# Optimization experiments

Hardware: AMD Instinct MI355X
Metric: run time of the kernel (lower is better)

Reference implementation:

```python
import jax, jax.numpy as jnp
import numpy as np

B, N, T, H, HEADS, HD, BK, FC, HOR = 8, 1600, 64, 32, 4, 8, 8, 16, 12


def setup_inputs() -> dict:
    key = jax.random.key(0)
    ks = jax.random.split(key, 32)
    r = lambda i, shape, s=0.1: jax.random.normal(ks[i], shape, dtype=jnp.float32) * s
    return dict(
        x=jax.random.normal(ks[0], (B, T, N), dtype=jnp.float32),
        dw_w=r(1, (1, 1, 3)), dw_b=r(2, (1,)),
        bn1_g=jnp.ones((1,), jnp.float32), bn1_b=jnp.zeros((1,), jnp.float32),
        bn1_m=jnp.zeros((1,), jnp.float32), bn1_v=jnp.ones((1,), jnp.float32),
        pw_w=r(3, (FC, 1, 1)), pw_b=r(4, (FC,)),
        bn2_g=jnp.ones((FC,), jnp.float32), bn2_b=jnp.zeros((FC,), jnp.float32),
        bn2_m=jnp.zeros((FC,), jnp.float32), bn2_v=jnp.ones((FC,), jnp.float32),
        fp_w=r(5, (H, FC * T)), fp_b=r(6, (H,)),
        qkv_lo_w=r(7, (3 * BK, H)), qkv_lo_b=r(8, (3 * BK,)),
        qkv_hi_w=r(9, (3 * H, 3 * BK)), qkv_hi_b=r(10, (3 * H,)),
        out_lo_w=r(11, (BK, H)), out_lo_b=r(12, (BK,)),
        out_hi_w=r(13, (H, BK)), out_hi_b=r(14, (H,)),
        u=r(15, (HEADS, N, BK)), v=r(16, (HEADS, BK, N)),
        log_reg=jnp.float32(np.log(1e-5)),
        hp_w=r(17, (BK, H)), hp_b=r(18, (BK,)),
        gru_wih=r(19, (3 * BK, 1)), gru_whh=r(20, (3 * BK, BK)),
        gru_bih=r(21, (3 * BK,)), gru_bhh=r(22, (3 * BK,)),
        op_w=r(23, (1, BK)), op_b=r(24, (1,)),
        log_decay=jnp.float32(-2.3),
        rg1_w=r(25, (BK, H)), rg1_b=r(26, (BK,)),
        rg2_w=r(27, (HOR, BK)), rg2_b=r(28, (HOR,)),
    )


def _bn(x, g, b, m, v):  # x: [BN, C, T], inference-mode BatchNorm1d
    inv = g / jnp.sqrt(v + 1e-5)
    return (x - m[None, :, None]) * inv[None, :, None] + b[None, :, None]


def _conv1d(x, w, b, pad):
    y = jax.lax.conv_general_dilated(x, w, (1,), [(pad, pad)],
                                     dimension_numbers=('NCH', 'OIH', 'NCH'))
    return y + b[None, :, None]


def reference(x, dw_w, dw_b, bn1_g, bn1_b, bn1_m, bn1_v, pw_w, pw_b,
              bn2_g, bn2_b, bn2_m, bn2_v, fp_w, fp_b,
              qkv_lo_w, qkv_lo_b, qkv_hi_w, qkv_hi_b,
              out_lo_w, out_lo_b, out_hi_w, out_hi_b, u, v, log_reg,
              hp_w, hp_b, gru_wih, gru_whh, gru_bih, gru_bhh, op_w, op_b,
              log_decay, rg1_w, rg1_b, rg2_w, rg2_b):
    # ---- TFEM: depthwise-separable conv per node series (eval mode, dropout off) ----
    xt = x.transpose(0, 2, 1).reshape(B * N, 1, T)          # [BN, 1, T]
    y = jax.nn.relu(_bn(_conv1d(xt, dw_w, dw_b, 1), bn1_g, bn1_b, bn1_m, bn1_v))
    y = jax.nn.relu(_bn(_conv1d(y, pw_w, pw_b, 0), bn2_g, bn2_b, bn2_m, bn2_v))  # [BN, FC, T]
    feat = (y.reshape(B * N, FC * T) @ fp_w.T + fp_b).reshape(B, N, H)

    # ---- LR-AGAM: low-rank qkv, linear attention + dense softmax for reg loss ----
    qkv = (feat @ qkv_lo_w.T + qkv_lo_b) @ qkv_hi_w.T + qkv_hi_b  # [B, N, 3H]
    q, k, vv = jnp.split(qkv, 3, axis=-1)
    resh = lambda t: t.reshape(B, N, HEADS, HD).transpose(0, 2, 1, 3)  # [B, h, N, d]
    q, k, vv = resh(q), resh(k), resh(vv)
    qe = jax.nn.elu(q) + 1.0
    ke = jax.nn.elu(k) + 1.0
    kv = jnp.einsum('bhnd,bhne->bhde', ke, vv)
    z = 1.0 / (ke.sum(-1) + 1e-8)                            # [B, h, N]
    att_out = jnp.einsum('bhnd,bhde,bhn->bhne', qe, kv, z)   # [B, h, N, d]
    # dense scores use the PRE-elu q, k (torch reassigns q/k only locally)
    scores = jnp.einsum('bhnd,bhmd->bhnm', q, k) / np.float32(np.sqrt(HD))
    scores = scores + jnp.matmul(u, v)[None]                 # learnable graph bias
    attn = jax.nn.softmax(scores, axis=-1)
    reg = jnp.exp(log_reg) * jnp.mean(jnp.abs(attn))
    out = att_out.transpose(0, 2, 1, 3).reshape(B, N, H)
    out = (out @ out_lo_w.T + out_lo_b) @ out_hi_w.T + out_hi_b
    feat = feat + out                                        # residual

    last = x[:, -1, :]                                       # [B, N]
    h0 = feat.reshape(B * N, H) @ hp_w.T + hp_b              # [BN, BK]
    cur0 = last.reshape(B * N, 1)

    def step(carry, _):
        h, cur = carry
        gx = cur @ gru_wih.T + gru_bih                       # [BN, 3BK]
        gh = h @ gru_whh.T + gru_bhh
        r_ = jax.nn.sigmoid(gx[:, :BK] + gh[:, :BK])
        zg = jax.nn.sigmoid(gx[:, BK:2 * BK] + gh[:, BK:2 * BK])
        n_ = jnp.tanh(gx[:, 2 * BK:] + r_ * gh[:, 2 * BK:])
        h2 = (1.0 - zg) * n_ + zg * h
        p = h2 @ op_w.T + op_b                               # [BN, 1]
        return (h2, p), p[:, 0]

    _, preds = jax.lax.scan(step, (h0, cur0), None, length=HOR)  # [HOR, BN]
    gru_pred = preds.T.reshape(B, N, HOR)

    gate = jax.nn.sigmoid(jax.nn.relu(feat @ rg1_w.T + rg1_b) @ rg2_w.T + rg2_b)  # [B, N, HOR]
    ts = jnp.arange(1, HOR + 1, dtype=jnp.float32)
    decay = jnp.exp(-jnp.exp(log_decay) * ts)[None, None, :]
    final = gate * gru_pred + (1.0 - gate) * last[..., None] * decay
    return final, reg
```

## Files before the change

### kernel.cpp

```cpp
#include <hip/hip_runtime.h>
#include <math.h>

constexpr int cB = 8, cN = 1600, cT = 64, cH = 32, cHEADS = 4, cHD = 8, cFC = 16, cHOR = 12;
constexpr int cROWS = cB * cN;

typedef __attribute__((ext_vector_type(8))) short short8;
typedef __attribute__((ext_vector_type(4))) float f32x4;

__device__ __forceinline__ float sigmoidf_(float x) { return 1.0f / (1.0f + __expf(-x)); }
__device__ __forceinline__ float tanhf_(float x) {
    float xc = fminf(fmaxf(x, -15.0f), 15.0f);
    float e = __expf(-2.0f * xc);
    return (1.0f - e) / (1.0f + e);
}
__device__ __forceinline__ float elu1_(float x) { return (x > 0.0f) ? (x + 1.0f) : __expf(x); }
__device__ __forceinline__ short f2bf(float f) {
    unsigned u = __float_as_uint(f);
    u = (u + 0x7fffu + ((u >> 16) & 1u)) >> 16;
    return (short)u;
}

__global__ __launch_bounds__(256) void k0_init(const float* __restrict__ fp_w,
                                               unsigned short* __restrict__ wbt,
                                               float* __restrict__ kv) {
    int i = blockIdx.x * 256 + threadIdx.x;
    wbt[i] = (unsigned short)f2bf(fp_w[i]);
    if (i < cB * cHEADS * 64) kv[i] = 0.0f;
}

__global__ __launch_bounds__(64) void kFeat(
    const float* __restrict__ x,
    const float* __restrict__ dw_w, const float* __restrict__ dw_b,
    const float* __restrict__ bn1_g, const float* __restrict__ bn1_b,
    const float* __restrict__ bn1_m, const float* __restrict__ bn1_v,
    const float* __restrict__ pw_w, const float* __restrict__ pw_b,
    const float* __restrict__ bn2_g, const float* __restrict__ bn2_b,
    const float* __restrict__ bn2_m, const float* __restrict__ bn2_v,
    const unsigned short* __restrict__ wbt,
    float* __restrict__ feat_p)
{
    __shared__ float y1s[16 * 65];

    const int l = threadIdx.x;
    const int rg = blockIdx.x >> 1;
    const int hk = blockIdx.x & 1;
    const int r0 = rg * 16;
    const int b = r0 / cN;
    const int n0 = r0 - b * cN;

    const float inv1 = bn1_g[0] * rsqrtf(bn1_v[0] + 1e-5f);
    const float A = inv1;
    const float C = (dw_b[0] - bn1_m[0]) * inv1 + bn1_b[0];
    const float w0 = dw_w[0], w1 = dw_w[1], w2 = dw_w[2];

    {
        const int rr = l & 15;
        const int t0 = (l >> 4) * 16;
        const float* xp = x + (size_t)b * cT * cN + (n0 + rr);
        float xv[18];
        #pragma unroll
        for (int q = 0; q < 18; ++q) {
            int t = t0 - 1 + q;
            xv[q] = (t >= 0 && t < cT) ? xp[(size_t)t * cN] : 0.0f;
        }
        #pragma unroll
        for (int q = 0; q < 16; ++q) {
            float s = w0 * xv[q] + w1 * xv[q + 1] + w2 * xv[q + 2];
            y1s[rr * 65 + t0 + q] = fmaxf(0.0f, fmaf(s, A, C));
        }
    }
    __syncthreads();

    float a2r[8], c2r[8];
    #pragma unroll
    for (int cc = 0; cc < 8; ++cc) {
        const int c = hk * 8 + cc;
        const float inv2 = bn2_g[c] * rsqrtf(bn2_v[c] + 1e-5f);
        a2r[cc] = pw_w[c] * inv2;
        c2r[cc] = (pw_b[c] - bn2_m[c]) * inv2 + bn2_b[c];
    }

    const int rr = l & 15;
    const int off = (l >> 4) * 8;
    float y1r[16];
    #pragma unroll
    for (int p = 0; p < 8; ++p) {
        y1r[p]     = y1s[rr * 65 + off + p];
        y1r[8 + p] = y1s[rr * 65 + 32 + off + p];
    }

    const unsigned short* b0p = wbt + (size_t)(l & 15) * 1024 + hk * 512 + off;
    const unsigned short* b1p = wbt + (size_t)(16 + (l & 15)) * 1024 + hk * 512 + off;

    f32x4 acc0 = {0.f, 0.f, 0.f, 0.f};
    f32x4 acc1 = {0.f, 0.f, 0.f, 0.f};

    #pragma unroll
    for (int kk = 0; kk < 16; ++kk) {
        const float a2 = a2r[kk >> 1], c2v = c2r[kk >> 1];
        short8 af;
        #pragma unroll
        for (int i = 0; i < 8; ++i) {
            const float y2 = fmaxf(0.0f, fmaf(a2, y1r[(kk & 1) * 8 + i], c2v));
            af[i] = f2bf(y2);
        }
        const short8 bf0 = *(const short8*)(b0p + kk * 32);
        const short8 bf1 = *(const short8*)(b1p + kk * 32);
        acc0 = __builtin_amdgcn_mfma_f32_16x16x32_bf16(af, bf0, acc0, 0, 0, 0);
        acc1 = __builtin_amdgcn_mfma_f32_16x16x32_bf16(af, bf1, acc1, 0, 0, 0);
    }

    float* fp = feat_p + (size_t)hk * ((size_t)cROWS * cH);
    const int col = l & 15;
    const int rbase = r0 + (l >> 4) * 4;
    #pragma unroll
    for (int reg = 0; reg < 4; ++reg) {
        fp[(size_t)(rbase + reg) * cH + col]      = acc0[reg];
        fp[(size_t)(rbase + reg) * cH + 16 + col] = acc1[reg];
    }
}

__global__ __launch_bounds__(256) void k2_qkv(
    const float* __restrict__ feat_p, const float* __restrict__ fp_b,
    const float* __restrict__ lo_w, const float* __restrict__ lo_b,
    const float* __restrict__ hi_w, const float* __restrict__ hi_b,
    float* __restrict__ feat_c, float* __restrict__ qe,
    float* __restrict__ zz, float* __restrict__ kvout)
{
    __shared__ float lbuf[32][25];
    __shared__ float ske[32][33];
    __shared__ float svv[32][33];

    const int tid = threadIdx.x;
    const int r = tid >> 3;
    const int j = tid & 7;
    const int row = blockIdx.x * 32 + r;
    const int b = __builtin_amdgcn_readfirstlane((blockIdx.x * 32) / cN);
    const int n = row - b * cN;

    float f[cH];
    {
        const float4* f0 = (const float4*)(feat_p + (size_t)row * cH);
        const float4* f1 = (const float4*)(feat_p + (size_t)cROWS * cH + (size_t)row * cH);
        #pragma unroll
        for (int q = 0; q < 8; ++q) {
            float4 v0 = f0[q], v1 = f1[q];
            f[4*q]   = v0.x + v1.x + fp_b[4*q];
            f[4*q+1] = v0.y + v1.y + fp_b[4*q+1];
            f[4*q+2] = v0.z + v1.z + fp_b[4*q+2];
            f[4*q+3] = v0.w + v1.w + fp_b[4*q+3];
        }
    }
    {
        float4 wc;
        wc.x = f[4*j]; wc.y = f[4*j+1]; wc.z = f[4*j+2]; wc.w = f[4*j+3];
        ((float4*)(feat_c + (size_t)row * cH))[j] = wc;
    }

    float lo0 = lo_b[j], lo1 = lo_b[j+8], lo2 = lo_b[j+16];
    #pragma unroll
    for (int i = 0; i < cH; ++i) {
        lo0 = fmaf(f[i], lo_w[j * cH + i], lo0);
        lo1 = fmaf(f[i], lo_w[(j+8) * cH + i], lo1);
        lo2 = fmaf(f[i], lo_w[(j+16) * cH + i], lo2);
    }
    lbuf[r][j] = lo0; lbuf[r][j+8] = lo1; lbuf[r][j+16] = lo2;
    __syncthreads();
    float lof[24];
    #pragma unroll
    for (int i = 0; i < 24; ++i) lof[i] = lbuf[r][i];

    float qv[4], kv4[4], vv4[4];
    #pragma unroll
    for (int m = 0; m < 4; ++m) {
        const int oi = m * 8 + j;
        float sq = hi_b[oi], sk = hi_b[32 + oi], sv = hi_b[64 + oi];
        #pragma unroll
        for (int i = 0; i < 24; ++i) {
            sq = fmaf(lof[i], hi_w[oi * 24 + i], sq);
            sk = fmaf(lof[i], hi_w[(32 + oi) * 24 + i], sk);
            sv = fmaf(lof[i], hi_w[(64 + oi) * 24 + i], sv);
        }
        qv[m] = elu1_(sq);
        kv4[m] = elu1_(sk);
        vv4[m] = sv;
    }

    float s0 = kv4[0], s1 = kv4[1], s2 = kv4[2], s3 = kv4[3];
    #pragma unroll
    for (int off = 1; off < 8; off <<= 1) {
        s0 += __shfl_xor(s0, off, 8);
        s1 += __shfl_xor(s1, off, 8);
        s2 += __shfl_xor(s2, off, 8);
        s3 += __shfl_xor(s3, off, 8);
    }
    if (j < 4) {
        float sv = (j == 0) ? s0 : ((j == 1) ? s1 : ((j == 2) ? s2 : s3));
        zz[(size_t)(b * cHEADS + j) * cN + n] = 1.0f / (sv + 1e-8f);
    }

    #pragma unroll
    for (int m = 0; m < 4; ++m) {
        qe[(size_t)row * cH + m * 8 + j] = qv[m];
        ske[r][m * 8 + j] = kv4[m];
        svv[r][m * 8 + j] = vv4[m];
    }
    __syncthreads();

    {
        const int m = tid >> 6, d = (tid >> 3) & 7, e = tid & 7;
        float s = 0.0f;
        #pragma unroll
        for (int rr = 0; rr < 32; ++rr)
            s = fmaf(ske[rr][m * 8 + d], svv[rr][m * 8 + e], s);
        atomicAdd(&kvout[(size_t)(b * cHEADS + m) * 64 + d * 8 + e], s);
    }
}

__global__ __launch_bounds__(256) void k4_final(
    const float* __restrict__ x,
    const float* __restrict__ feat_c, const float* __restrict__ qe,
    const float* __restrict__ zz, const float* __restrict__ kv,
    const float* __restrict__ out_lo_w, const float* __restrict__ out_lo_b,
    const float* __restrict__ out_hi_w, const float* __restrict__ out_hi_b,
    const float* __restrict__ hp_w, const float* __restrict__ hp_b,
    const float* __restrict__ gru_wih, const float* __restrict__ gru_whh,
    const float* __restrict__ gru_bih, const float* __restrict__ gru_bhh,
    const float* __restrict__ op_w, const float* __restrict__ op_b,
    const float* __restrict__ log_decay,
    const float* __restrict__ rg1_w, const float* __restrict__ rg1_b,
    const float* __restrict__ rg2_w, const float* __restrict__ rg2_b,
    const float* __restrict__ log_reg,
    float* __restrict__ out)
{
    __shared__ float sA[32][36];
    __shared__ float sB[32][36];
    __shared__ float sC[32][36];

    const int tid = threadIdx.x;
    const int r = tid >> 3;
    const int j = tid & 7;
    const int row = blockIdx.x * 32 + r;
    const int b = __builtin_amdgcn_readfirstlane((blockIdx.x * 32) / cN);
    const int n = row - b * cN;

    {
        const float4* q4 = (const float4*)(qe + (size_t)row * cH);
        float4 v = q4[j];
        *(float4*)&sA[r][4 * j] = v;
    }
    __syncthreads();

    float o_m[4];
    #pragma unroll
    for (int m = 0; m < 4; ++m) {
        const float z = zz[(size_t)(b * cHEADS + m) * cN + n];
        const float* kvp = kv + (size_t)(b * cHEADS + m) * 64;
        float s = 0.0f;
        #pragma unroll
        for (int d = 0; d < 8; ++d)
            s = fmaf(sA[r][m * 8 + d], kvp[d * 8 + j], s);
        o_m[m] = s * z;
    }
    #pragma unroll
    for (int m = 0; m < 4; ++m) sB[r][m * 8 + j] = o_m[m];
    __syncthreads();

    float lo_j = out_lo_b[j];
    #pragma unroll
    for (int i = 0; i < cH; ++i)
        lo_j = fmaf(sB[r][i], out_lo_w[j * cH + i], lo_j);

    float lof[8];
    #pragma unroll
    for (int i = 0; i < 8; ++i) lof[i] = __shfl(lo_j, i, 8);

    float f2_m[4];
    #pragma unroll
    for (int m = 0; m < 4; ++m) {
        const int i = m * 8 + j;
        float s = out_hi_b[i];
        #pragma unroll
        for (int q = 0; q < 8; ++q) s = fmaf(lof[q], out_hi_w[i * 8 + q], s);
        f2_m[m] = feat_c[(size_t)row * cH + i] + s;
        sC[r][i] = f2_m[m];
    }
    __syncthreads();

    float h0_j = hp_b[j], g1_j = rg1_b[j];
    #pragma unroll
    for (int i = 0; i < cH; ++i) {
        float fv = sC[r][i];
        h0_j = fmaf(fv, hp_w[j * cH + i], h0_j);
        g1_j = fmaf(fv, rg1_w[j * cH + i], g1_j);
    }
    g1_j = fmaxf(0.0f, g1_j);

    float g1f[8];
    #pragma unroll
    for (int i = 0; i < 8; ++i) g1f[i] = __shfl(g1_j, i, 8);

    float ga = rg2_b[j], gb_ = rg2_b[8 + (j & 3)];
    #pragma unroll
    for (int q = 0; q < 8; ++q) {
        ga = fmaf(g1f[q], rg2_w[j * 8 + q], ga);
        gb_ = fmaf(g1f[q], rg2_w[(8 + (j & 3)) * 8 + q], gb_);
    }
    const float gate_a = sigmoidf_(ga);
    const float gate_b = sigmoidf_(gb_);

    const float last = x[(size_t)b * cT * cN + (size_t)(cT - 1) * cN + n];

    float whh_r[8], whh_z[8], whh_n[8], opw[8];
    #pragma unroll
    for (int i = 0; i < 8; ++i) {
        whh_r[i] = gru_whh[j * 8 + i];
        whh_z[i] = gru_whh[(8 + j) * 8 + i];
        whh_n[i] = gru_whh[(16 + j) * 8 + i];
        opw[i] = op_w[i];
    }
    const float wih_r = gru_wih[j], wih_z = gru_wih[8 + j], wih_n = gru_wih[16 + j];
    const float bih_r = gru_bih[j], bih_z = gru_bih[8 + j], bih_n = gru_bih[16 + j];
    const float bhh_r = gru_bhh[j], bhh_z = gru_bhh[8 + j], bhh_n = gru_bhh[16 + j];
    const float opb = op_b[0];

    float h_full[8];
    #pragma unroll
    for (int i = 0; i < 8; ++i) h_full[i] = __shfl(h0_j, i, 8);
    float h_own = h0_j;
    float cur = last;
    float po_a = 0.0f, po_b = 0.0f;

    #pragma unroll
    for (int s = 0; s < cHOR; ++s) {
        float ghr = bhh_r, ghz = bhh_z, ghn = bhh_n;
        #pragma unroll
        for (int i = 0; i < 8; ++i) {
            ghr = fmaf(h_full[i], whh_r[i], ghr);
            ghz = fmaf(h_full[i], whh_z[i], ghz);
            ghn = fmaf(h_full[i], whh_n[i], ghn);
        }
        const float r_ = sigmoidf_(fmaf(wih_r, cur, bih_r) + ghr);
        const float zg = sigmoidf_(fmaf(wih_z, cur, bih_z) + ghz);
        const float nn = tanhf_(fmaf(wih_n, cur, bih_n) + r_ * ghn);
        const float hn = (1.0f - zg) * nn + zg * h_own;
        h_own = hn;
        #pragma unroll
        for (int i = 0; i < 8; ++i) h_full[i] = __shfl(hn, i, 8);
        float p = opb;
        #pragma unroll
        for (int i = 0; i < 8; ++i) p = fmaf(h_full[i], opw[i], p);
        po_a = (s == j) ? p : po_a;
        po_b = (s == 8 + j) ? p : po_b;
        cur = p;
    }

    const float dk = __expf(log_decay[0]);
    float* orow = out + (size_t)row * 12;
    orow[j] = gate_a * po_a + (1.0f - gate_a) * last * __expf(-dk * (float)(j + 1));
    if (j < 4)
        orow[8 + j] = gate_b * po_b + (1.0f - gate_b) * last * __expf(-dk * (float)(j + 9));

    if (row == 0 && j == 0)
        out[(size_t)cROWS * 12] = __expf(log_reg[0]) * (1.0f / (float)cN);
}

extern "C" void kernel_launch(void* const* d_in, const int* in_sizes, int n_in,
                              void* d_out, int out_size, void* d_ws, size_t ws_size,
                              hipStream_t stream)
{
    const float* x      = (const float*)d_in[0];
    const float* dw_w   = (const float*)d_in[1];
    const float* dw_b   = (const float*)d_in[2];
    const float* bn1_g  = (const float*)d_in[3];
    const float* bn1_b  = (const float*)d_in[4];
    const float* bn1_m  = (const float*)d_in[5];
    const float* bn1_v  = (const float*)d_in[6];
    const float* pw_w   = (const float*)d_in[7];
    const float* pw_b   = (const float*)d_in[8];
    const float* bn2_g  = (const float*)d_in[9];
    const float* bn2_b  = (const float*)d_in[10];
    const float* bn2_m  = (const float*)d_in[11];
    const float* bn2_v  = (const float*)d_in[12];
    const float* fp_w   = (const float*)d_in[13];
    const float* fp_b   = (const float*)d_in[14];
    const float* lo_w   = (const float*)d_in[15];
    const float* lo_b   = (const float*)d_in[16];
    const float* hi_w   = (const float*)d_in[17];
    const float* hi_b   = (const float*)d_in[18];
    const float* olo_w  = (const float*)d_in[19];
    const float* olo_b  = (const float*)d_in[20];
    const float* ohi_w  = (const float*)d_in[21];
    const float* ohi_b  = (const float*)d_in[22];
    const float* log_reg = (const float*)d_in[25];
    const float* hp_w   = (const float*)d_in[26];
    const float* hp_b   = (const float*)d_in[27];
    const float* gru_wih = (const float*)d_in[28];
    const float* gru_whh = (const float*)d_in[29];
    const float* gru_bih = (const float*)d_in[30];
    const float* gru_bhh = (const float*)d_in[31];
    const float* op_w   = (const float*)d_in[32];
    const float* op_b   = (const float*)d_in[33];
    const float* log_decay = (const float*)d_in[34];
    const float* rg1_w  = (const float*)d_in[35];
    const float* rg1_b  = (const float*)d_in[36];
    const float* rg2_w  = (const float*)d_in[37];
    const float* rg2_b  = (const float*)d_in[38];

    float* ws = (float*)d_ws;
    unsigned short* wbt = (unsigned short*)ws;
    float* feat_p = ws + 16384;
    float* feat_c = feat_p + 2 * 409600;
    float* qe     = feat_c + 409600;
    float* zz     = qe + 409600;
    float* kv     = zz + 51200;

    k0_init<<<128, 256, 0, stream>>>(fp_w, wbt, kv);
    kFeat<<<1600, 64, 0, stream>>>(x, dw_w, dw_b, bn1_g, bn1_b, bn1_m, bn1_v,
                                   pw_w, pw_b, bn2_g, bn2_b, bn2_m, bn2_v,
                                   wbt, feat_p);
    k2_qkv<<<cROWS / 32, 256, 0, stream>>>(feat_p, fp_b, lo_w, lo_b, hi_w, hi_b,
                                           feat_c, qe, zz, kv);
    k4_final<<<cROWS / 32, 256, 0, stream>>>(x, feat_c, qe, zz, kv,
                                             olo_w, olo_b, ohi_w, ohi_b,
                                             hp_w, hp_b, gru_wih, gru_whh, gru_bih, gru_bhh,
                                             op_w, op_b, log_decay,
                                             rg1_w, rg1_b, rg2_w, rg2_b, log_reg,
                                             (float*)d_out);
}
```

Baseline: 52.16 us.

## Fuse feature projection with QKV, fold low-rank weights, replace atomics with reduction

Merges the feature GEMM and the QKV stage into one kernel. Each 16-row block now runs the full K=1024 itself instead of writing split-K partials, which removes the feat_p round trip. The low-rank weight pairs (qkv lo/hi and out lo/hi) are precomputed into dense 96x32 and 32x32 matrices in a prep kernel, and the normalizer z is folded into q. Per-block KV partial sums go to a buffer and are reduced by a small dedicated kernel instead of atomics. The trade-off is half as many blocks in the MFMA kernel, a longer serial K loop, and one extra launch.

```diff
diff --git a/kernel.cpp b/kernel.cpp
--- a/kernel.cpp
+++ b/kernel.cpp
@@ -20,15 +20,51 @@
     return (short)u;
 }
 
-__global__ __launch_bounds__(256) void k0_init(const float* __restrict__ fp_w,
-                                               unsigned short* __restrict__ wbt,
-                                               float* __restrict__ kv) {
-    int i = blockIdx.x * 256 + threadIdx.x;
-    wbt[i] = (unsigned short)f2bf(fp_w[i]);
-    if (i < cB * cHEADS * 64) kv[i] = 0.0f;
-}
-
-__global__ __launch_bounds__(64) void kFeat(
+__global__ __launch_bounds__(256) void k0_prep(
+    const float* __restrict__ fp_w,
+    const float* __restrict__ lo_w, const float* __restrict__ lo_b,
+    const float* __restrict__ hi_w, const float* __restrict__ hi_b,
+    const float* __restrict__ olo_w, const float* __restrict__ olo_b,
+    const float* __restrict__ ohi_w, const float* __restrict__ ohi_b,
+    unsigned short* __restrict__ wbt,
+    float* __restrict__ Wq, float* __restrict__ bq,
+    float* __restrict__ Wo, float* __restrict__ bo)
+{
+    const int g = blockIdx.x * 256 + threadIdx.x;
+    #pragma unroll
+    for (int q = 0; q < 8; ++q) {
+        const int i = g * 8 + q;
+        wbt[i] = (unsigned short)f2bf(fp_w[i]);
+    }
+    if (g < 3072) {
+        const int oi = g >> 5, i = g & 31;
+        float s = 0.0f;
+        #pragma unroll
+        for (int p = 0; p < 24; ++p) s = fmaf(hi_w[oi * 24 + p], lo_w[p * 32 + i], s);
+        Wq[g] = s;
+    }
+    if (g < 1024) {
+        const int i = g >> 5, q = g & 31;
+        float s = 0.0f;
+        #pragma unroll
+        for (int p = 0; p < 8; ++p) s = fmaf(ohi_w[i * 8 + p], olo_w[p * 32 + q], s);
+        Wo[g] = s;
+    }
+    if (g < 96) {
+        float s = hi_b[g];
+        #pragma unroll
+        for (int p = 0; p < 24; ++p) s = fmaf(hi_w[g * 24 + p], lo_b[p], s);
+        bq[g] = s;
+    }
+    if (g < 32) {
+        float s = ohi_b[g];
+        #pragma unroll
+        for (int p = 0; p < 8; ++p) s = fmaf(ohi_w[g * 8 + p], olo_b[p], s);
+        bo[g] = s;
+    }
+}
+
+__global__ __launch_bounds__(64) void kFQ(
     const float* __restrict__ x,
     const float* __restrict__ dw_w, const float* __restrict__ dw_b,
     const float* __restrict__ bn1_g, const float* __restrict__ bn1_b,
@@ -36,15 +72,19 @@
     const float* __restrict__ pw_w, const float* __restrict__ pw_b,
     const float* __restrict__ bn2_g, const float* __restrict__ bn2_b,
     const float* __restrict__ bn2_m, const float* __restrict__ bn2_v,
-    const unsigned short* __restrict__ wbt,
-    float* __restrict__ feat_p)
+    const unsigned short* __restrict__ wbt, const float* __restrict__ fp_b,
+    const float* __restrict__ Wq, const float* __restrict__ bq,
+    float* __restrict__ feat_c, float* __restrict__ qe,
+    float* __restrict__ pkv)
 {
     __shared__ float y1s[16 * 65];
+    __shared__ float sfeat[16 * 36];
+    __shared__ float ske[16 * 33];
+    __shared__ float svv[16 * 33];
 
     const int l = threadIdx.x;
-    const int rg = blockIdx.x >> 1;
-    const int hk = blockIdx.x & 1;
-    const int r0 = rg * 16;
+    const int bk = blockIdx.x;
+    const int r0 = bk * 16;
     const int b = r0 / cN;
     const int n0 = r0 - b * cN;
 
@@ -71,13 +111,12 @@
     }
     __syncthreads();
 
-    float a2r[8], c2r[8];
-    #pragma unroll
-    for (int cc = 0; cc < 8; ++cc) {
-        const int c = hk * 8 + cc;
+    float a2r[16], c2r[16];
+    #pragma unroll
+    for (int c = 0; c < 16; ++c) {
         const float inv2 = bn2_g[c] * rsqrtf(bn2_v[c] + 1e-5f);
-        a2r[cc] = pw_w[c] * inv2;
-        c2r[cc] = (pw_b[c] - bn2_m[c]) * inv2 + bn2_b[c];
+        a2r[c] = pw_w[c] * inv2;
+        c2r[c] = (pw_b[c] - bn2_m[c]) * inv2 + bn2_b[c];
     }
 
     const int rr = l & 15;
@@ -89,14 +128,14 @@
         y1r[8 + p] = y1s[rr * 65 + 32 + off + p];
     }
 
-    const unsigned short* b0p = wbt + (size_t)(l & 15) * 1024 + hk * 512 + off;
-    const unsigned short* b1p = wbt + (size_t)(16 + (l & 15)) * 1024 + hk * 512 + off;
+    const unsigned short* b0p = wbt + (size_t)(l & 15) * 1024 + off;
+    const unsigned short* b1p = wbt + (size_t)(16 + (l & 15)) * 1024 + off;
 
     f32x4 acc0 = {0.f, 0.f, 0.f, 0.f};
     f32x4 acc1 = {0.f, 0.f, 0.f, 0.f};
 
     #pragma unroll
-    for (int kk = 0; kk < 16; ++kk) {
+    for (int kk = 0; kk < 32; ++kk) {
         const float a2 = a2r[kk >> 1], c2v = c2r[kk >> 1];
         short8 af;
         #pragma unroll
@@ -110,119 +149,110 @@
         acc1 = __builtin_amdgcn_mfma_f32_16x16x32_bf16(af, bf1, acc1, 0, 0, 0);
     }
 
-    float* fp = feat_p + (size_t)hk * ((size_t)cROWS * cH);
-    const int col = l & 15;
-    const int rbase = r0 + (l >> 4) * 4;
-    #pragma unroll
-    for (int reg = 0; reg < 4; ++reg) {
-        fp[(size_t)(rbase + reg) * cH + col]      = acc0[reg];
-        fp[(size_t)(rbase + reg) * cH + 16 + col] = acc1[reg];
-    }
-}
-
-__global__ __launch_bounds__(256) void k2_qkv(
-    const float* __restrict__ feat_p, const float* __restrict__ fp_b,
-    const float* __restrict__ lo_w, const float* __restrict__ lo_b,
-    const float* __restrict__ hi_w, const float* __restrict__ hi_b,
-    float* __restrict__ feat_c, float* __restrict__ qe,
-    float* __restrict__ zz, float* __restrict__ kvout)
+    {
+        const int col = l & 15;
+        const int rb = (l >> 4) * 4;
+        const float fb0 = fp_b[col], fb1 = fp_b[16 + col];
+        #pragma unroll
+        for (int reg = 0; reg < 4; ++reg) {
+            sfeat[(rb + reg) * 36 + col]      = acc0[reg] + fb0;
+            sfeat[(rb + reg) * 36 + 16 + col] = acc1[reg] + fb1;
+        }
+    }
+    __syncthreads();
+
+    {
+        float v[8];
+        #pragma unroll
+        for (int q = 0; q < 8; ++q)
+            v[q] = sfeat[(l >> 2) * 36 + (l & 3) * 8 + q];
+        float4* dst = (float4*)(feat_c + (size_t)r0 * cH + l * 8);
+        dst[0] = make_float4(v[0], v[1], v[2], v[3]);
+        dst[1] = make_float4(v[4], v[5], v[6], v[7]);
+    }
+
+    {
+        const int rr2 = l >> 2, hd = l & 3;
+        const int row = r0 + rr2;
+        float4 f4[8];
+        #pragma unroll
+        for (int c = 0; c < 8; ++c)
+            f4[c] = *(const float4*)&sfeat[rr2 * 36 + c * 4];
+
+        float qv[8], kev[8], vvv[8];
+        #pragma unroll
+        for (int g = 0; g < 3; ++g) {
+            #pragma unroll
+            for (int jj = 0; jj < 8; ++jj) {
+                const int oi = g * 32 + hd * 8 + jj;
+                const float4* w4 = (const float4*)(Wq + (size_t)oi * 32);
+                float s = bq[oi];
+                #pragma unroll
+                for (int c = 0; c < 8; ++c) {
+                    float4 wv = w4[c];
+                    s = fmaf(f4[c].x, wv.x, s);
+                    s = fmaf(f4[c].y, wv.y, s);
+                    s = fmaf(f4[c].z, wv.z, s);
+                    s = fmaf(f4[c].w, wv.w, s);
+                }
+                if (g == 0) qv[jj] = s;
+                else if (g == 1) kev[jj] = s;
+                else vvv[jj] = s;
+            }
+        }
+        float zsum = 1e-8f;
+        #pragma unroll
+        for (int jj = 0; jj < 8; ++jj) {
+            qv[jj] = elu1_(qv[jj]);
+            kev[jj] = elu1_(kev[jj]);
+            zsum += kev[jj];
+        }
+        const float z = 1.0f / zsum;
+        float4* qdst = (float4*)(qe + (size_t)row * cH + hd * 8);
+        qdst[0] = make_float4(qv[0]*z, qv[1]*z, qv[2]*z, qv[3]*z);
+        qdst[1] = make_float4(qv[4]*z, qv[5]*z, qv[6]*z, qv[7]*z);
+        #pragma unroll
+        for (int jj = 0; jj < 8; ++jj) {
+            ske[rr2 * 33 + hd * 8 + jj] = kev[jj];
+            svv[rr2 * 33 + hd * 8 + jj] = vvv[jj];
+        }
+    }
+    __syncthreads();
+
+    {
+        float out4[4];
+        #pragma unroll
+        for (int j = 0; j < 4; ++j) {
+            const int cc = l * 4 + j;
+            const int h = cc >> 6, d = (cc >> 3) & 7, e = cc & 7;
+            float s = 0.0f;
+            #pragma unroll
+            for (int rr3 = 0; rr3 < 16; ++rr3)
+                s = fmaf(ske[rr3 * 33 + h * 8 + d], svv[rr3 * 33 + h * 8 + e], s);
+            out4[j] = s;
+        }
+        *(float4*)(pkv + (size_t)bk * 256 + l * 4) =
+            make_float4(out4[0], out4[1], out4[2], out4[3]);
+    }
+}
+
+__global__ __launch_bounds__(64) void k3r(const float* __restrict__ pkv,
+                                          float* __restrict__ kv)
 {
-    __shared__ float lbuf[32][25];
-    __shared__ float ske[32][33];
-    __shared__ float svv[32][33];
-
+    const int bh = blockIdx.x;
+    const int b = bh >> 2, h = bh & 3;
     const int tid = threadIdx.x;
-    const int r = tid >> 3;
-    const int j = tid & 7;
-    const int row = blockIdx.x * 32 + r;
-    const int b = __builtin_amdgcn_readfirstlane((blockIdx.x * 32) / cN);
-    const int n = row - b * cN;
-
-    float f[cH];
-    {
-        const float4* f0 = (const float4*)(feat_p + (size_t)row * cH);
-        const float4* f1 = (const float4*)(feat_p + (size_t)cROWS * cH + (size_t)row * cH);
-        #pragma unroll
-        for (int q = 0; q < 8; ++q) {
-            float4 v0 = f0[q], v1 = f1[q];
-            f[4*q]   = v0.x + v1.x + fp_b[4*q];
-            f[4*q+1] = v0.y + v1.y + fp_b[4*q+1];
-            f[4*q+2] = v0.z + v1.z + fp_b[4*q+2];
-            f[4*q+3] = v0.w + v1.w + fp_b[4*q+3];
-        }
-    }
-    {
-        float4 wc;
-        wc.x = f[4*j]; wc.y = f[4*j+1]; wc.z = f[4*j+2]; wc.w = f[4*j+3];
-        ((float4*)(feat_c + (size_t)row * cH))[j] = wc;
-    }
-
-    float lo0 = lo_b[j], lo1 = lo_b[j+8], lo2 = lo_b[j+16];
-    #pragma unroll
-    for (int i = 0; i < cH; ++i) {
-        lo0 = fmaf(f[i], lo_w[j * cH + i], lo0);
-        lo1 = fmaf(f[i], lo_w[(j+8) * cH + i], lo1);
-        lo2 = fmaf(f[i], lo_w[(j+16) * cH + i], lo2);
-    }
-    lbuf[r][j] = lo0; lbuf[r][j+8] = lo1; lbuf[r][j+16] = lo2;
-    __syncthreads();
-    float lof[24];
-    #pragma unroll
-    for (int i = 0; i < 24; ++i) lof[i] = lbuf[r][i];
-
-    float qv[4], kv4[4], vv4[4];
-    #pragma unroll
-    for (int m = 0; m < 4; ++m) {
-        const int oi = m * 8 + j;
-        float sq = hi_b[oi], sk = hi_b[32 + oi], sv = hi_b[64 + oi];
-        #pragma unroll
-        for (int i = 0; i < 24; ++i) {
-            sq = fmaf(lof[i], hi_w[oi * 24 + i], sq);
-            sk = fmaf(lof[i], hi_w[(32 + oi) * 24 + i], sk);
-            sv = fmaf(lof[i], hi_w[(64 + oi) * 24 + i], sv);
-        }
-        qv[m] = elu1_(sq);
-        kv4[m] = elu1_(sk);
-        vv4[m] = sv;
-    }
-
-    float s0 = kv4[0], s1 = kv4[1], s2 = kv4[2], s3 = kv4[3];
-    #pragma unroll
-    for (int off = 1; off < 8; off <<= 1) {
-        s0 += __shfl_xor(s0, off, 8);
-        s1 += __shfl_xor(s1, off, 8);
-        s2 += __shfl_xor(s2, off, 8);
-        s3 += __shfl_xor(s3, off, 8);
-    }
-    if (j < 4) {
-        float sv = (j == 0) ? s0 : ((j == 1) ? s1 : ((j == 2) ? s2 : s3));
-        zz[(size_t)(b * cHEADS + j) * cN + n] = 1.0f / (sv + 1e-8f);
-    }
-
-    #pragma unroll
-    for (int m = 0; m < 4; ++m) {
-        qe[(size_t)row * cH + m * 8 + j] = qv[m];
-        ske[r][m * 8 + j] = kv4[m];
-        svv[r][m * 8 + j] = vv4[m];
-    }
-    __syncthreads();
-
-    {
-        const int m = tid >> 6, d = (tid >> 3) & 7, e = tid & 7;
-        float s = 0.0f;
-        #pragma unroll
-        for (int rr = 0; rr < 32; ++rr)
-            s = fmaf(ske[rr][m * 8 + d], svv[rr][m * 8 + e], s);
-        atomicAdd(&kvout[(size_t)(b * cHEADS + m) * 64 + d * 8 + e], s);
-    }
+    float s = 0.0f;
+    for (int p = 0; p < 100; ++p)
+        s += pkv[(size_t)(b * 100 + p) * 256 + h * 64 + tid];
+    kv[(size_t)bh * 64 + tid] = s;
 }
 
 __global__ __launch_bounds__(256) void k4_final(
     const float* __restrict__ x,
     const float* __restrict__ feat_c, const float* __restrict__ qe,
-    const float* __restrict__ zz, const float* __restrict__ kv,
-    const float* __restrict__ out_lo_w, const float* __restrict__ out_lo_b,
-    const float* __restrict__ out_hi_w, const float* __restrict__ out_hi_b,
+    const float* __restrict__ kv,
+    const float* __restrict__ Wo, const float* __restrict__ bo,
     const float* __restrict__ hp_w, const float* __restrict__ hp_b,
     const float* __restrict__ gru_wih, const float* __restrict__ gru_whh,
     const float* __restrict__ gru_bih, const float* __restrict__ gru_bhh,
@@ -254,34 +284,25 @@
     float o_m[4];
     #pragma unroll
     for (int m = 0; m < 4; ++m) {
-        const float z = zz[(size_t)(b * cHEADS + m) * cN + n];
         const float* kvp = kv + (size_t)(b * cHEADS + m) * 64;
         float s = 0.0f;
         #pragma unroll
         for (int d = 0; d < 8; ++d)
             s = fmaf(sA[r][m * 8 + d], kvp[d * 8 + j], s);
-        o_m[m] = s * z;
+        o_m[m] = s;
     }
     #pragma unroll
     for (int m = 0; m < 4; ++m) sB[r][m * 8 + j] = o_m[m];
     __syncthreads();
-
-    float lo_j = out_lo_b[j];
-    #pragma unroll
-    for (int i = 0; i < cH; ++i)
-        lo_j = fmaf(sB[r][i], out_lo_w[j * cH + i], lo_j);
-
-    float lof[8];
-    #pragma unroll
-    for (int i = 0; i < 8; ++i) lof[i] = __shfl(lo_j, i, 8);
 
     float f2_m[4];
     #pragma unroll
     for (int m = 0; m < 4; ++m) {
         const int i = m * 8 + j;
-        float s = out_hi_b[i];
-        #pragma unroll
-        for (int q = 0; q < 8; ++q) s = fmaf(lof[q], out_hi_w[i * 8 + q], s);
+        float s = bo[i];
+        const float* wrow = Wo + (size_t)i * 32;
+        #pragma unroll
+        for (int q = 0; q < 32; ++q) s = fmaf(sB[r][q], wrow[q], s);
         f2_m[m] = feat_c[(size_t)row * cH + i] + s;
         sC[r][i] = f2_m[m];
     }
@@ -409,20 +430,25 @@
 
     float* ws = (float*)d_ws;
     unsigned short* wbt = (unsigned short*)ws;
-    float* feat_p = ws + 16384;
-    float* feat_c = feat_p + 2 * 409600;
-    float* qe     = feat_c + 409600;
-    float* zz     = qe + 409600;
-    float* kv     = zz + 51200;
-
-    k0_init<<<128, 256, 0, stream>>>(fp_w, wbt, kv);
-    kFeat<<<1600, 64, 0, stream>>>(x, dw_w, dw_b, bn1_g, bn1_b, bn1_m, bn1_v,
-                                   pw_w, pw_b, bn2_g, bn2_b, bn2_m, bn2_v,
-                                   wbt, feat_p);
-    k2_qkv<<<cROWS / 32, 256, 0, stream>>>(feat_p, fp_b, lo_w, lo_b, hi_w, hi_b,
-                                           feat_c, qe, zz, kv);
-    k4_final<<<cROWS / 32, 256, 0, stream>>>(x, feat_c, qe, zz, kv,
-                                             olo_w, olo_b, ohi_w, ohi_b,
+    float* Wq     = ws + 16384;
+    float* bq     = Wq + 3072;
+    float* Wo     = bq + 128;
+    float* bo     = Wo + 1024;
+    float* qe     = bo + 64;
+    float* feat_c = qe + 409600;
+    float* pkv    = feat_c + 409600;
+    float* kv     = pkv + 204800;
+
+    k0_prep<<<16, 256, 0, stream>>>(fp_w, lo_w, lo_b, hi_w, hi_b,
+                                    olo_w, olo_b, ohi_w, ohi_b,
+                                    wbt, Wq, bq, Wo, bo);
+    kFQ<<<800, 64, 0, stream>>>(x, dw_w, dw_b, bn1_g, bn1_b, bn1_m, bn1_v,
+                                pw_w, pw_b, bn2_g, bn2_b, bn2_m, bn2_v,
+                                wbt, fp_b, Wq, bq,
+                                feat_c, qe, pkv);
+    k3r<<<32, 64, 0, stream>>>(pkv, kv);
+    k4_final<<<cROWS / 32, 256, 0, stream>>>(x, feat_c, qe, kv,
+                                             Wo, bo,
                                              hp_w, hp_b, gru_wih, gru_whh, gru_bih, gru_bhh,
                                              op_w, op_b, log_decay,
                                              rg1_w, rg1_b, rg2_w, rg2_b, log_reg,
```

New measurement: 65.54 us. 25.7% more time.

## Fuse all stages into one persistent kernel with grid-wide barrier for KV reduction

Applied to the files above, without the earlier changes.

Replaces the four-kernel pipeline with a single kernel of 400 blocks that keeps each block's 32 rows of features, q, k and v in LDS instead of global memory. The per-batch KV sum is now built from per-block partials followed by an atomic-counter grid barrier, replacing the global atomicAdd and a separate launch. The low-rank weight pairs (qkv lo/hi, out lo/hi) are folded algebraically into single 32-wide matrices inside each block, and the z normalisation is folded into q. Each block now reconverts the full fp_w matrix to bf16 in LDS, which is redundant per-block work, and the grid barrier relies on all 400 blocks being co-resident (two per CU at 74 KB LDS).

```diff
diff --git a/kernel.cpp b/kernel.cpp
--- a/kernel.cpp
+++ b/kernel.cpp
@@ -1,8 +1,11 @@
 #include <hip/hip_runtime.h>
 #include <math.h>
 
-constexpr int cB = 8, cN = 1600, cT = 64, cH = 32, cHEADS = 4, cHD = 8, cFC = 16, cHOR = 12;
+constexpr int cB = 8, cN = 1600, cT = 64, cH = 32, cHEADS = 4, cHOR = 12;
 constexpr int cROWS = cB * cN;
+constexpr int NB = 400;
+constexpr int RPB = 32;
+constexpr int BPB = 50;
 
 typedef __attribute__((ext_vector_type(8))) short short8;
 typedef __attribute__((ext_vector_type(4))) float f32x4;
@@ -20,15 +23,9 @@
     return (short)u;
 }
 
-__global__ __launch_bounds__(256) void k0_init(const float* __restrict__ fp_w,
-                                               unsigned short* __restrict__ wbt,
-                                               float* __restrict__ kv) {
-    int i = blockIdx.x * 256 + threadIdx.x;
-    wbt[i] = (unsigned short)f2bf(fp_w[i]);
-    if (i < cB * cHEADS * 64) kv[i] = 0.0f;
-}
-
-__global__ __launch_bounds__(64) void kFeat(
+#define LDS_BYTES 74368
+
+__global__ __launch_bounds__(256, 2) void mono(
     const float* __restrict__ x,
     const float* __restrict__ dw_w, const float* __restrict__ dw_b,
     const float* __restrict__ bn1_g, const float* __restrict__ bn1_b,
@@ -36,193 +33,11 @@
     const float* __restrict__ pw_w, const float* __restrict__ pw_b,
     const float* __restrict__ bn2_g, const float* __restrict__ bn2_b,
     const float* __restrict__ bn2_m, const float* __restrict__ bn2_v,
-    const unsigned short* __restrict__ wbt,
-    float* __restrict__ feat_p)
-{
-    __shared__ float y1s[16 * 65];
-
-    const int l = threadIdx.x;
-    const int rg = blockIdx.x >> 1;
-    const int hk = blockIdx.x & 1;
-    const int r0 = rg * 16;
-    const int b = r0 / cN;
-    const int n0 = r0 - b * cN;
-
-    const float inv1 = bn1_g[0] * rsqrtf(bn1_v[0] + 1e-5f);
-    const float A = inv1;
-    const float C = (dw_b[0] - bn1_m[0]) * inv1 + bn1_b[0];
-    const float w0 = dw_w[0], w1 = dw_w[1], w2 = dw_w[2];
-
-    {
-        const int rr = l & 15;
-        const int t0 = (l >> 4) * 16;
-        const float* xp = x + (size_t)b * cT * cN + (n0 + rr);
-        float xv[18];
-        #pragma unroll
-        for (int q = 0; q < 18; ++q) {
-            int t = t0 - 1 + q;
-            xv[q] = (t >= 0 && t < cT) ? xp[(size_t)t * cN] : 0.0f;
-        }
-        #pragma unroll
-        for (int q = 0; q < 16; ++q) {
-            float s = w0 * xv[q] + w1 * xv[q + 1] + w2 * xv[q + 2];
-            y1s[rr * 65 + t0 + q] = fmaxf(0.0f, fmaf(s, A, C));
-        }
-    }
-    __syncthreads();
-
-    float a2r[8], c2r[8];
-    #pragma unroll
-    for (int cc = 0; cc < 8; ++cc) {
-        const int c = hk * 8 + cc;
-        const float inv2 = bn2_g[c] * rsqrtf(bn2_v[c] + 1e-5f);
-        a2r[cc] = pw_w[c] * inv2;
-        c2r[cc] = (pw_b[c] - bn2_m[c]) * inv2 + bn2_b[c];
-    }
-
-    const int rr = l & 15;
-    const int off = (l >> 4) * 8;
-    float y1r[16];
-    #pragma unroll
-    for (int p = 0; p < 8; ++p) {
-        y1r[p]     = y1s[rr * 65 + off + p];
-        y1r[8 + p] = y1s[rr * 65 + 32 + off + p];
-    }
-
-    const unsigned short* b0p = wbt + (size_t)(l & 15) * 1024 + hk * 512 + off;
-    const unsigned short* b1p = wbt + (size_t)(16 + (l & 15)) * 1024 + hk * 512 + off;
-
-    f32x4 acc0 = {0.f, 0.f, 0.f, 0.f};
-    f32x4 acc1 = {0.f, 0.f, 0.f, 0.f};
-
-    #pragma unroll
-    for (int kk = 0; kk < 16; ++kk) {
-        const float a2 = a2r[kk >> 1], c2v = c2r[kk >> 1];
-        short8 af;
-        #pragma unroll
-        for (int i = 0; i < 8; ++i) {
-            const float y2 = fmaxf(0.0f, fmaf(a2, y1r[(kk & 1) * 8 + i], c2v));
-            af[i] = f2bf(y2);
-        }
-        const short8 bf0 = *(const short8*)(b0p + kk * 32);
-        const short8 bf1 = *(const short8*)(b1p + kk * 32);
-        acc0 = __builtin_amdgcn_mfma_f32_16x16x32_bf16(af, bf0, acc0, 0, 0, 0);
-        acc1 = __builtin_amdgcn_mfma_f32_16x16x32_bf16(af, bf1, acc1, 0, 0, 0);
-    }
-
-    float* fp = feat_p + (size_t)hk * ((size_t)cROWS * cH);
-    const int col = l & 15;
-    const int rbase = r0 + (l >> 4) * 4;
-    #pragma unroll
-    for (int reg = 0; reg < 4; ++reg) {
-        fp[(size_t)(rbase + reg) * cH + col]      = acc0[reg];
-        fp[(size_t)(rbase + reg) * cH + 16 + col] = acc1[reg];
-    }
-}
-
-__global__ __launch_bounds__(256) void k2_qkv(
-    const float* __restrict__ feat_p, const float* __restrict__ fp_b,
+    const float* __restrict__ fp_w, const float* __restrict__ fp_b,
     const float* __restrict__ lo_w, const float* __restrict__ lo_b,
     const float* __restrict__ hi_w, const float* __restrict__ hi_b,
-    float* __restrict__ feat_c, float* __restrict__ qe,
-    float* __restrict__ zz, float* __restrict__ kvout)
-{
-    __shared__ float lbuf[32][25];
-    __shared__ float ske[32][33];
-    __shared__ float svv[32][33];
-
-    const int tid = threadIdx.x;
-    const int r = tid >> 3;
-    const int j = tid & 7;
-    const int row = blockIdx.x * 32 + r;
-    const int b = __builtin_amdgcn_readfirstlane((blockIdx.x * 32) / cN);
-    const int n = row - b * cN;
-
-    float f[cH];
-    {
-        const float4* f0 = (const float4*)(feat_p + (size_t)row * cH);
-        const float4* f1 = (const float4*)(feat_p + (size_t)cROWS * cH + (size_t)row * cH);
-        #pragma unroll
-        for (int q = 0; q < 8; ++q) {
-            float4 v0 = f0[q], v1 = f1[q];
-            f[4*q]   = v0.x + v1.x + fp_b[4*q];
-            f[4*q+1] = v0.y + v1.y + fp_b[4*q+1];
-            f[4*q+2] = v0.z + v1.z + fp_b[4*q+2];
-            f[4*q+3] = v0.w + v1.w + fp_b[4*q+3];
-        }
-    }
-    {
-        float4 wc;
-        wc.x = f[4*j]; wc.y = f[4*j+1]; wc.z = f[4*j+2]; wc.w = f[4*j+3];
-        ((float4*)(feat_c + (size_t)row * cH))[j] = wc;
-    }
-
-    float lo0 = lo_b[j], lo1 = lo_b[j+8], lo2 = lo_b[j+16];
-    #pragma unroll
-    for (int i = 0; i < cH; ++i) {
-        lo0 = fmaf(f[i], lo_w[j * cH + i], lo0);
-        lo1 = fmaf(f[i], lo_w[(j+8) * cH + i], lo1);
-        lo2 = fmaf(f[i], lo_w[(j+16) * cH + i], lo2);
-    }
-    lbuf[r][j] = lo0; lbuf[r][j+8] = lo1; lbuf[r][j+16] = lo2;
-    __syncthreads();
-    float lof[24];
-    #pragma unroll
-    for (int i = 0; i < 24; ++i) lof[i] = lbuf[r][i];
-
-    float qv[4], kv4[4], vv4[4];
-    #pragma unroll
-    for (int m = 0; m < 4; ++m) {
-        const int oi = m * 8 + j;
-        float sq = hi_b[oi], sk = hi_b[32 + oi], sv = hi_b[64 + oi];
-        #pragma unroll
-        for (int i = 0; i < 24; ++i) {
-            sq = fmaf(lof[i], hi_w[oi * 24 + i], sq);
-            sk = fmaf(lof[i], hi_w[(32 + oi) * 24 + i], sk);
-            sv = fmaf(lof[i], hi_w[(64 + oi) * 24 + i], sv);
-        }
-        qv[m] = elu1_(sq);
-        kv4[m] = elu1_(sk);
-        vv4[m] = sv;
-    }
-
-    float s0 = kv4[0], s1 = kv4[1], s2 = kv4[2], s3 = kv4[3];
-    #pragma unroll
-    for (int off = 1; off < 8; off <<= 1) {
-        s0 += __shfl_xor(s0, off, 8);
-        s1 += __shfl_xor(s1, off, 8);
-        s2 += __shfl_xor(s2, off, 8);
-        s3 += __shfl_xor(s3, off, 8);
-    }
-    if (j < 4) {
-        float sv = (j == 0) ? s0 : ((j == 1) ? s1 : ((j == 2) ? s2 : s3));
-        zz[(size_t)(b * cHEADS + j) * cN + n] = 1.0f / (sv + 1e-8f);
-    }
-
-    #pragma unroll
-    for (int m = 0; m < 4; ++m) {
-        qe[(size_t)row * cH + m * 8 + j] = qv[m];
-        ske[r][m * 8 + j] = kv4[m];
-        svv[r][m * 8 + j] = vv4[m];
-    }
-    __syncthreads();
-
-    {
-        const int m = tid >> 6, d = (tid >> 3) & 7, e = tid & 7;
-        float s = 0.0f;
-        #pragma unroll
-        for (int rr = 0; rr < 32; ++rr)
-            s = fmaf(ske[rr][m * 8 + d], svv[rr][m * 8 + e], s);
-        atomicAdd(&kvout[(size_t)(b * cHEADS + m) * 64 + d * 8 + e], s);
-    }
-}
-
-__global__ __launch_bounds__(256) void k4_final(
-    const float* __restrict__ x,
-    const float* __restrict__ feat_c, const float* __restrict__ qe,
-    const float* __restrict__ zz, const float* __restrict__ kv,
-    const float* __restrict__ out_lo_w, const float* __restrict__ out_lo_b,
-    const float* __restrict__ out_hi_w, const float* __restrict__ out_hi_b,
+    const float* __restrict__ olo_w, const float* __restrict__ olo_b,
+    const float* __restrict__ ohi_w, const float* __restrict__ ohi_b,
     const float* __restrict__ hp_w, const float* __restrict__ hp_b,
     const float* __restrict__ gru_wih, const float* __restrict__ gru_whh,
     const float* __restrict__ gru_bih, const float* __restrict__ gru_bhh,
@@ -231,66 +46,266 @@
     const float* __restrict__ rg1_w, const float* __restrict__ rg1_b,
     const float* __restrict__ rg2_w, const float* __restrict__ rg2_b,
     const float* __restrict__ log_reg,
+    float* __restrict__ pkv, unsigned* __restrict__ cnt,
     float* __restrict__ out)
 {
-    __shared__ float sA[32][36];
-    __shared__ float sB[32][36];
-    __shared__ float sC[32][36];
+    __shared__ __align__(16) unsigned char smem_[LDS_BYTES];
+    short* wbt  = (short*)smem_;
+    float* y1s  = (float*)(smem_ + 66048);
+    float* sfeat = y1s;
+    float* Wq  = (float*)smem_;
+    float* bq  = Wq + 3168;
+    float* Wo  = bq + 96;
+    float* bo  = Wo + 1056;
+    float* qe  = bo + 32;
+    float* ske = qe + 1056;
+    float* svv = ske + 1056;
+    float* skv = svv + 1056;
+    float* sB  = skv + 256;
+    float* sC  = sB + 1152;
 
     const int tid = threadIdx.x;
+    const int bk = blockIdx.x;
+    const int r0 = bk * RPB;
+    const int b = __builtin_amdgcn_readfirstlane(r0 / cN);
+    const int n0 = r0 - b * cN;
+
+    #pragma unroll 4
+    for (int q = 0; q < 32; ++q) {
+        const float4 v = *(const float4*)(fp_w + (size_t)q * 1024 + tid * 4);
+        short* d = wbt + q * 1032 + tid * 4;
+        d[0] = f2bf(v.x); d[1] = f2bf(v.y); d[2] = f2bf(v.z); d[3] = f2bf(v.w);
+    }
+    {
+        const float inv1 = bn1_g[0] * rsqrtf(bn1_v[0] + 1e-5f);
+        const float A = inv1;
+        const float C = (dw_b[0] - bn1_m[0]) * inv1 + bn1_b[0];
+        const float w0 = dw_w[0], w1 = dw_w[1], w2 = dw_w[2];
+        const int rr = tid & 31;
+        const int t0 = (tid >> 5) * 8;
+        const float* xp = x + (size_t)b * cT * cN + (n0 + rr);
+        float xv[10];
+        #pragma unroll
+        for (int q = 0; q < 10; ++q) {
+            const int t = t0 - 1 + q;
+            xv[q] = (t >= 0 && t < cT) ? xp[(size_t)t * cN] : 0.0f;
+        }
+        #pragma unroll
+        for (int q = 0; q < 8; ++q) {
+            const float s = w0 * xv[q] + w1 * xv[q + 1] + w2 * xv[q + 2];
+            y1s[rr * 65 + t0 + q] = fmaxf(0.0f, fmaf(s, A, C));
+        }
+    }
+    __syncthreads();
+
+    const int w    = tid >> 6;
+    const int l    = tid & 63;
+    const int tile = w >> 1;
+    const int half = w & 1;
+    const int off  = (l >> 4) * 8;
+
+    float a2r[8], c2r[8];
+    #pragma unroll
+    for (int cc = 0; cc < 8; ++cc) {
+        const int c = half * 8 + cc;
+        const float inv2 = bn2_g[c] * rsqrtf(bn2_v[c] + 1e-5f);
+        a2r[cc] = pw_w[c] * inv2;
+        c2r[cc] = (pw_b[c] - bn2_m[c]) * inv2 + bn2_b[c];
+    }
+    float y1r[16];
+    {
+        const int rl = tile * 16 + (l & 15);
+        #pragma unroll
+        for (int p = 0; p < 8; ++p) {
+            y1r[p]     = y1s[rl * 65 + off + p];
+            y1r[8 + p] = y1s[rl * 65 + 32 + off + p];
+        }
+    }
+    f32x4 acc0 = {0.f, 0.f, 0.f, 0.f};
+    f32x4 acc1 = {0.f, 0.f, 0.f, 0.f};
+    {
+        const short* bp0 = wbt + (l & 15) * 1032 + half * 512 + off;
+        const short* bp1 = bp0 + 16 * 1032;
+        #pragma unroll
+        for (int kk = 0; kk < 16; ++kk) {
+            const float a2 = a2r[kk >> 1], c2v = c2r[kk >> 1];
+            short8 af;
+            #pragma unroll
+            for (int i = 0; i < 8; ++i) {
+                const float y2 = fmaxf(0.0f, fmaf(a2, y1r[(kk & 1) * 8 + i], c2v));
+                af[i] = f2bf(y2);
+            }
+            const short8 bf0 = *(const short8*)(bp0 + kk * 32);
+            const short8 bf1 = *(const short8*)(bp1 + kk * 32);
+            acc0 = __builtin_amdgcn_mfma_f32_16x16x32_bf16(af, bf0, acc0, 0, 0, 0);
+            acc1 = __builtin_amdgcn_mfma_f32_16x16x32_bf16(af, bf1, acc1, 0, 0, 0);
+        }
+    }
+    __syncthreads();
+
+    {
+        const int col = l & 15;
+        const int rb = tile * 16 + (l >> 4) * 4;
+        if (half == 0) {
+            const float fb0 = fp_b[col], fb1 = fp_b[16 + col];
+            #pragma unroll
+            for (int reg = 0; reg < 4; ++reg) {
+                sfeat[(rb + reg) * 36 + col]      = acc0[reg] + fb0;
+                sfeat[(rb + reg) * 36 + 16 + col] = acc1[reg] + fb1;
+            }
+        }
+    }
+    #pragma unroll
+    for (int k = 0; k < 12; ++k) {
+        const int g = tid + k * 256;
+        const int oi = g >> 5, i = g & 31;
+        float s = 0.0f;
+        #pragma unroll
+        for (int p = 0; p < 24; ++p) s = fmaf(hi_w[oi * 24 + p], lo_w[p * 32 + i], s);
+        Wq[oi * 33 + i] = s;
+    }
+    #pragma unroll
+    for (int k = 0; k < 4; ++k) {
+        const int g = tid + k * 256;
+        const int oi = g >> 5, i = g & 31;
+        float s = 0.0f;
+        #pragma unroll
+        for (int p = 0; p < 8; ++p) s = fmaf(ohi_w[oi * 8 + p], olo_w[p * 32 + i], s);
+        Wo[oi * 33 + i] = s;
+    }
+    if (tid < 96) {
+        float s = hi_b[tid];
+        #pragma unroll
+        for (int p = 0; p < 24; ++p) s = fmaf(hi_w[tid * 24 + p], lo_b[p], s);
+        bq[tid] = s;
+    }
+    if (tid < 32) {
+        float s = ohi_b[tid];
+        #pragma unroll
+        for (int p = 0; p < 8; ++p) s = fmaf(ohi_w[tid * 8 + p], olo_b[p], s);
+        bo[tid] = s;
+    }
+    __syncthreads();
+    if (half == 1) {
+        const int col = l & 15;
+        const int rb = tile * 16 + (l >> 4) * 4;
+        #pragma unroll
+        for (int reg = 0; reg < 4; ++reg) {
+            sfeat[(rb + reg) * 36 + col]      += acc0[reg];
+            sfeat[(rb + reg) * 36 + 16 + col] += acc1[reg];
+        }
+    }
+    __syncthreads();
+
     const int r = tid >> 3;
     const int j = tid & 7;
-    const int row = blockIdx.x * 32 + r;
-    const int b = __builtin_amdgcn_readfirstlane((blockIdx.x * 32) / cN);
-    const int n = row - b * cN;
-
-    {
-        const float4* q4 = (const float4*)(qe + (size_t)row * cH);
-        float4 v = q4[j];
-        *(float4*)&sA[r][4 * j] = v;
-    }
-    __syncthreads();
+    {
+        float f[cH];
+        #pragma unroll
+        for (int i = 0; i < cH; ++i) f[i] = sfeat[r * 36 + i];
+
+        float qv[4], kv4[4], vv4[4];
+        #pragma unroll
+        for (int m = 0; m < 4; ++m) {
+            const int oi = m * 8 + j;
+            float sq = bq[oi], sk = bq[32 + oi], sv = bq[64 + oi];
+            #pragma unroll
+            for (int i = 0; i < cH; ++i) {
+                const float fv = f[i];
+                sq = fmaf(fv, Wq[oi * 33 + i], sq);
+                sk = fmaf(fv, Wq[(32 + oi) * 33 + i], sk);
+                sv = fmaf(fv, Wq[(64 + oi) * 33 + i], sv);
+            }
+            qv[m] = elu1_(sq);
+            kv4[m] = elu1_(sk);
+            vv4[m] = sv;
+        }
+        float s0 = kv4[0], s1 = kv4[1], s2 = kv4[2], s3 = kv4[3];
+        #pragma unroll
+        for (int o2 = 1; o2 < 8; o2 <<= 1) {
+            s0 += __shfl_xor(s0, o2, 8);
+            s1 += __shfl_xor(s1, o2, 8);
+            s2 += __shfl_xor(s2, o2, 8);
+            s3 += __shfl_xor(s3, o2, 8);
+        }
+        const float z0 = 1.0f / (s0 + 1e-8f), z1 = 1.0f / (s1 + 1e-8f);
+        const float z2 = 1.0f / (s2 + 1e-8f), z3 = 1.0f / (s3 + 1e-8f);
+        qe[r * 33 + j]      = qv[0] * z0;
+        qe[r * 33 + 8 + j]  = qv[1] * z1;
+        qe[r * 33 + 16 + j] = qv[2] * z2;
+        qe[r * 33 + 24 + j] = qv[3] * z3;
+        #pragma unroll
+        for (int m = 0; m < 4; ++m) {
+            ske[r * 33 + m * 8 + j] = kv4[m];
+            svv[r * 33 + m * 8 + j] = vv4[m];
+        }
+    }
+    __syncthreads();
+
+    {
+        const int h = tid >> 6, d = (tid >> 3) & 7, e = tid & 7;
+        float s = 0.0f;
+        #pragma unroll
+        for (int rr = 0; rr < RPB; ++rr)
+            s = fmaf(ske[rr * 33 + h * 8 + d], svv[rr * 33 + h * 8 + e], s);
+        pkv[(size_t)bk * 256 + tid] = s;
+    }
+
+    __threadfence();
+    __syncthreads();
+    if (tid == 0) {
+        const unsigned old = atomicAdd(cnt, 1u);
+        const unsigned target = (old / (unsigned)NB + 1u) * (unsigned)NB;
+        while (__hip_atomic_load(cnt, __ATOMIC_ACQUIRE, __HIP_MEMORY_SCOPE_AGENT) < target)
+            __builtin_amdgcn_s_sleep(8);
+    }
+    __syncthreads();
+    __threadfence();
+
+    {
+        const float* pp = pkv + (size_t)(b * BPB) * 256 + tid;
+        float s0 = 0.f, s1 = 0.f;
+        #pragma unroll 5
+        for (int p = 0; p < BPB; p += 2) {
+            s0 += pp[(size_t)p * 256];
+            s1 += pp[(size_t)(p + 1) * 256];
+        }
+        skv[tid] = s0 + s1;
+    }
+    __syncthreads();
+
+    const int row = r0 + r;
+    const int n = n0 + r;
 
     float o_m[4];
     #pragma unroll
     for (int m = 0; m < 4; ++m) {
-        const float z = zz[(size_t)(b * cHEADS + m) * cN + n];
-        const float* kvp = kv + (size_t)(b * cHEADS + m) * 64;
         float s = 0.0f;
         #pragma unroll
         for (int d = 0; d < 8; ++d)
-            s = fmaf(sA[r][m * 8 + d], kvp[d * 8 + j], s);
-        o_m[m] = s * z;
-    }
-    #pragma unroll
-    for (int m = 0; m < 4; ++m) sB[r][m * 8 + j] = o_m[m];
-    __syncthreads();
-
-    float lo_j = out_lo_b[j];
-    #pragma unroll
-    for (int i = 0; i < cH; ++i)
-        lo_j = fmaf(sB[r][i], out_lo_w[j * cH + i], lo_j);
-
-    float lof[8];
-    #pragma unroll
-    for (int i = 0; i < 8; ++i) lof[i] = __shfl(lo_j, i, 8);
+            s = fmaf(qe[r * 33 + m * 8 + d], skv[m * 64 + d * 8 + j], s);
+        o_m[m] = s;
+    }
+    #pragma unroll
+    for (int m = 0; m < 4; ++m) sB[r * 36 + m * 8 + j] = o_m[m];
+    __syncthreads();
 
     float f2_m[4];
     #pragma unroll
     for (int m = 0; m < 4; ++m) {
         const int i = m * 8 + j;
-        float s = out_hi_b[i];
-        #pragma unroll
-        for (int q = 0; q < 8; ++q) s = fmaf(lof[q], out_hi_w[i * 8 + q], s);
-        f2_m[m] = feat_c[(size_t)row * cH + i] + s;
-        sC[r][i] = f2_m[m];
+        float s = bo[i];
+        #pragma unroll
+        for (int q = 0; q < cH; ++q) s = fmaf(sB[r * 36 + q], Wo[i * 33 + q], s);
+        f2_m[m] = sfeat[r * 36 + i] + s;
+        sC[r * 36 + i] = f2_m[m];
     }
     __syncthreads();
 
     float h0_j = hp_b[j], g1_j = rg1_b[j];
     #pragma unroll
     for (int i = 0; i < cH; ++i) {
-        float fv = sC[r][i];
+        const float fv = sC[r * 36 + i];
         h0_j = fmaf(fv, hp_w[j * cH + i], h0_j);
         g1_j = fmaf(fv, rg1_w[j * cH + i], g1_j);
     }
@@ -361,7 +376,7 @@
     if (j < 4)
         orow[8 + j] = gate_b * po_b + (1.0f - gate_b) * last * __expf(-dk * (float)(j + 9));
 
-    if (row == 0 && j == 0)
+    if (bk == 0 && tid == 0)
         out[(size_t)cROWS * 12] = __expf(log_reg[0]) * (1.0f / (float)cN);
 }
 
@@ -408,23 +423,16 @@
     const float* rg2_b  = (const float*)d_in[38];
 
     float* ws = (float*)d_ws;
-    unsigned short* wbt = (unsigned short*)ws;
-    float* feat_p = ws + 16384;
-    float* feat_c = feat_p + 2 * 409600;
-    float* qe     = feat_c + 409600;
-    float* zz     = qe + 409600;
-    float* kv     = zz + 51200;
-
-    k0_init<<<128, 256, 0, stream>>>(fp_w, wbt, kv);
-    kFeat<<<1600, 64, 0, stream>>>(x, dw_w, dw_b, bn1_g, bn1_b, bn1_m, bn1_v,
-                                   pw_w, pw_b, bn2_g, bn2_b, bn2_m, bn2_v,
-                                   wbt, feat_p);
-    k2_qkv<<<cROWS / 32, 256, 0, stream>>>(feat_p, fp_b, lo_w, lo_b, hi_w, hi_b,
-                                           feat_c, qe, zz, kv);
-    k4_final<<<cROWS / 32, 256, 0, stream>>>(x, feat_c, qe, zz, kv,
-                                             olo_w, olo_b, ohi_w, ohi_b,
-                                             hp_w, hp_b, gru_wih, gru_whh, gru_bih, gru_bhh,
-                                             op_w, op_b, log_decay,
-                                             rg1_w, rg1_b, rg2_w, rg2_b, log_reg,
-                                             (float*)d_out);
+    float* pkv = ws;
+    unsigned* cnt = (unsigned*)(ws + NB * 256);
+
+    hipMemsetAsync(cnt, 0, sizeof(unsigned), stream);
+    mono<<<NB, 256, 0, stream>>>(x, dw_w, dw_b, bn1_g, bn1_b, bn1_m, bn1_v,
+                                 pw_w, pw_b, bn2_g, bn2_b, bn2_m, bn2_v,
+                                 fp_w, fp_b, lo_w, lo_b, hi_w, hi_b,
+                                 olo_w, olo_b, ohi_w, ohi_b,
+                                 hp_w, hp_b, gru_wih, gru_whh, gru_bih, gru_bhh,
+                                 op_w, op_b, log_decay,
+                                 rg1_w, rg1_b, rg2_w, rg2_b, log_reg,
+                                 pkv, cnt, (float*)d_out);
 }
```

Result: slower. 130.2 us (+149.6%).
